# Performance work log

Measured on AMD Instinct MI355X. Metric: run time of the kernel, lower is better.

Reference implementation:

```python
import jax, jax.numpy as jnp
import numpy as np

EPS = 1e-5
LAMBDA_REG = 1.0
ALPHA_ENTROPY = 0.5
ALPHA_DIVERSITY = 0.5

B, N, D, K = 32, 1024, 256, 512  # batch, tokens, dim_embed, num_embed


def setup_inputs() -> dict:
    key = jax.random.key(0)
    k0, k1, k2 = jax.random.split(key, 3)
    inputs = jax.random.normal(k0, (B, N, D), dtype=jnp.float32)
    gamma = jnp.ones((D,), jnp.float32)
    beta = jnp.zeros((D,), jnp.float32)
    # keras 'uniform' initializer default: U(-0.05, 0.05)
    embed_w = jax.random.uniform(k1, (D, K), jnp.float32, -0.05, 0.05)
    # keras 'random_normal' default: stddev=0.05
    d_w = jax.random.normal(k2, (D, D), jnp.float32) * 0.05
    d_b = jnp.zeros((D,), jnp.float32)
    return {"inputs": inputs, "gamma": gamma, "beta": beta,
            "embed_w": embed_w, "d_w": d_w, "d_b": d_b}


def _project_columns_to_simplex(P_sol):
    # P_sol: (K, M); project each column onto the probability simplex.
    P_t = P_sol.T                                   # (M, K)
    sorted_P = -jnp.sort(-P_t, axis=1)              # descending
    cumsum = jnp.cumsum(sorted_P, axis=1)
    k = jnp.arange(1, K + 1, dtype=P_t.dtype)
    thresholds = (cumsum - 1.0) / k
    valid = (sorted_P > thresholds).astype(jnp.int32)
    max_idx = jnp.argmax(valid * jnp.arange(K, dtype=jnp.int32), axis=1)  # (M,)
    sel_cumsum = jnp.take_along_axis(cumsum, max_idx[:, None], axis=1)[:, 0]
    theta = (sel_cumsum - 1.0) / (max_idx.astype(P_t.dtype) + 1.0)
    return jax.nn.relu(P_t - theta[:, None]).T      # (K, M)


def _forward(inputs, gamma, beta, embed_w, d_w, d_b):
    # dense + layernorm
    x = jnp.matmul(inputs, d_w) + d_b
    mean = jnp.mean(x, axis=-1, keepdims=True)
    var = jnp.var(x, axis=-1, keepdims=True)
    x = gamma * ((x - mean) / jnp.sqrt(var + EPS)) + beta

    flat = x.reshape(-1, D)                          # (M, D)
    flat_sg = jax.lax.stop_gradient(flat)

    # hard assignment (VQ-style, on detached encodings)
    dists = (jnp.sum(flat_sg ** 2, axis=1, keepdims=True)
             + jnp.sum(embed_w ** 2, axis=0, keepdims=True)
             - 2.0 * jnp.matmul(flat_sg, embed_w))   # (M, K)
    assign = jnp.argmin(dists, axis=1)
    P_tilde = jax.nn.one_hot(assign, K, dtype=jnp.float32).T  # (K, M)

    # regularized least squares: (C^T C + lam I) P = C^T Z + lam P_tilde
    C = embed_w                                       # (D, K)
    Z = flat.T                                        # (D, M)
    A = jnp.matmul(C.T, C) + LAMBDA_REG * jnp.eye(K, dtype=jnp.float32)
    b = jnp.matmul(C.T, Z) + LAMBDA_REG * P_tilde     # (K, M)
    P_sol = jnp.linalg.solve(A, b)
    P_proj = _project_columns_to_simplex(P_sol)       # (K, M)

    out_P_proj = P_proj.T.reshape(B, N, K)

    # perplexity
    p_j = jnp.mean(out_P_proj, axis=(0, 1))
    p_j = jnp.clip(p_j, 1e-10, 1.0 - 1e-9)
    p_j = p_j / jnp.sum(p_j)
    entropy_bits = -jnp.sum(p_j * jnp.log(p_j) / jnp.log(2.0))
    perplexity = jnp.power(2.0, entropy_bits)

    Zq_flat = jnp.matmul(C, P_proj).T                 # (M, D)

    # entropy regularizer
    p_mean = jnp.mean(out_P_proj, axis=(0, 1))
    p_mn = p_mean / (jnp.sum(p_mean) + EPS)
    entropy_reg = -jnp.sum(p_mn * jnp.log(p_mn + EPS))

    # diversity loss on l2-normalized codebook columns
    norm_cb = embed_w / jnp.sqrt(jnp.maximum(jnp.sum(embed_w ** 2, axis=0, keepdims=True), 1e-12))
    sims = jnp.matmul(norm_cb.T, norm_cb)
    masked = sims * (1.0 - jnp.eye(K, dtype=jnp.float32))
    diversity_loss = jnp.mean(jax.nn.relu(masked))

    primary_loss = jnp.mean((Zq_flat - flat) ** 2)  # discrete_loss=False path
    loss = primary_loss + ALPHA_ENTROPY * entropy_reg + ALPHA_DIVERSITY * diversity_loss

    Zq = Zq_flat.reshape(B, N, D)
    return Zq, out_P_proj, loss, perplexity


def reference(inputs, gamma, beta, embed_w, d_w, d_b):
    return _forward(inputs, gamma, beta, embed_w, d_w, d_b)
```

## Files before the change

kernel.cpp:

```cpp
#include <hip/hip_runtime.h>
#include <math.h>


#define M_ 32768
#define D_ 256
#define K_ 512
#define TAU 0.006f

typedef short bf16x8 __attribute__((ext_vector_type(8)));
typedef unsigned short u16x8 __attribute__((ext_vector_type(8)));
typedef unsigned short u16x4 __attribute__((ext_vector_type(4)));
typedef float f32x4 __attribute__((ext_vector_type(4)));

#define LSTR 56

__device__ inline void split_rne(float f, unsigned short& h, unsigned short& l)
{
    unsigned int u = __float_as_uint(f);
    unsigned int uh = u + (0x7FFFu + ((u >> 16) & 1u));
    h = (unsigned short)(uh >> 16);
    float fh = __uint_as_float(((unsigned int)h) << 16);
    float r = f - fh;
    l = (unsigned short)(__float_as_uint(r) >> 16);
}

__device__ inline unsigned short rne16(float f)
{
    unsigned int u = __float_as_uint(f);
    u += 0x7FFFu + ((u >> 16) & 1u);
    return (unsigned short)(u >> 16);
}

__device__ inline void stage16r(const float* __restrict__ g,
                                unsigned short* __restrict__ lh)
{
    unsigned short hi[16];
#pragma unroll
    for (int q = 0; q < 4; ++q) {
        float4 v = ((const float4*)g)[q];
        float f[4] = {v.x, v.y, v.z, v.w};
#pragma unroll
        for (int e = 0; e < 4; ++e) hi[q*4+e] = rne16(f[e]);
    }
    *(u16x8*)lh       = *(u16x8*)hi;
    *(u16x8*)(lh + 8) = *(u16x8*)(hi + 8);
}

template<int EPI, int AU16>
__global__ __launch_bounds__(256)
void mfma_gemm(const float* __restrict__ Af, const unsigned short* __restrict__ Ah,
               const unsigned short* __restrict__ Bh,
               float* __restrict__ Out, int Kd, int N,
               const float* __restrict__ AinvM, const int* __restrict__ assign,
               const float* Zref, float* __restrict__ lossPart)
{
    __shared__ unsigned short sA[128*LSTR];
    __shared__ unsigned short sB[128*LSTR];
    __shared__ float red[256];
    const int tid = threadIdx.x;
    const int m0 = blockIdx.y * 128, n0 = blockIdx.x * 128;
    const int w = tid >> 6, lane = tid & 63;
    const int wr = (w & 1) * 64, wc = (w >> 1) * 64;
    const int cg = lane >> 4, cr = lane & 15;

    f32x4 acc[4][4];
    const f32x4 z4 = {0.f, 0.f, 0.f, 0.f};
#pragma unroll
    for (int i = 0; i < 4; ++i)
#pragma unroll
        for (int j = 0; j < 4; ++j) acc[i][j] = z4;

    const int sr = tid >> 1;
    const int sk = (tid & 1) * 16;
    const int soff = sr * LSTR + sk;
    const unsigned short* Bgh = Bh + (size_t)(n0 + sr) * Kd + sk;

    for (int kb = 0; kb < Kd; kb += 32) {
        if (AU16) {
            const unsigned short* Agh = Ah + (size_t)(m0 + sr) * Kd + sk + kb;
            *(u16x8*)&sA[soff]     = *(const u16x8*)(Agh);
            *(u16x8*)&sA[soff + 8] = *(const u16x8*)(Agh + 8);
        } else {
            stage16r(Af + (size_t)(m0 + sr) * Kd + sk + kb, sA + soff);
        }
        *(u16x8*)&sB[soff]     = *(const u16x8*)(Bgh + kb);
        *(u16x8*)&sB[soff + 8] = *(const u16x8*)(Bgh + kb + 8);
        __syncthreads();
        bf16x8 ah[4], bh[4];
#pragma unroll
        for (int f = 0; f < 4; ++f) {
            ah[f] = *(const bf16x8*)&sA[(wr + f*16 + cr) * LSTR + cg*8];
            bh[f] = *(const bf16x8*)&sB[(wc + f*16 + cr) * LSTR + cg*8];
        }
#pragma unroll
        for (int i = 0; i < 4; ++i)
#pragma unroll
            for (int j = 0; j < 4; ++j)
                acc[i][j] = __builtin_amdgcn_mfma_f32_16x16x32_bf16(ah[i], bh[j], acc[i][j], 0, 0, 0);
        __syncthreads();
    }

    if (EPI == 2) {
#pragma unroll
        for (int i = 0; i < 4; ++i) {
#pragma unroll
            for (int q = 0; q < 4; ++q) {
                const int row = m0 + wr + i*16 + cg*4 + q;
                const int am = assign[row];
                const float* Arow = AinvM + (size_t)am * K_ + n0 + wc;
#pragma unroll
                for (int j = 0; j < 4; ++j)
                    Out[(size_t)row * N + n0 + wc + j*16 + cr] =
                        acc[i][j][q] + Arow[j*16 + cr];
            }
        }
    } else {
        float lsum = 0.f;
#pragma unroll
        for (int i = 0; i < 4; ++i) {
#pragma unroll
            for (int q = 0; q < 4; ++q) {
                const int row = m0 + wr + i*16 + cg*4 + q;
#pragma unroll
                for (int j = 0; j < 4; ++j) {
                    const int col = n0 + wc + j*16 + cr;
                    const float v = acc[i][j][q];
                    const float zv = Zref[(size_t)row * N + col];
                    const float d = v - zv;
                    lsum += d * d;
                    Out[(size_t)row * N + col] = v;
                }
            }
        }
        red[tid] = lsum;
        __syncthreads();
        for (int s = 128; s > 0; s >>= 1) {
            if (tid < s) red[tid] += red[tid + s];
            __syncthreads();
        }
        if (tid == 0) lossPart[blockIdx.y * gridDim.x + blockIdx.x] = red[0];
    }
}

__global__ __launch_bounds__(256)
void score_mfma_argmin(const unsigned short* __restrict__ Zh, const unsigned short* __restrict__ Zl,
                       const unsigned short* __restrict__ Bth, const unsigned short* __restrict__ Btl,
                       const float* __restrict__ cn2, const float* __restrict__ zn2,
                       float* __restrict__ PV, float* __restrict__ PB,
                       int* __restrict__ PI)
{
    __shared__ unsigned short sAh[128*LSTR], sAl[128*LSTR];
    __shared__ unsigned short sBh[128*LSTR], sBl[128*LSTR];
    __shared__ float l1v[128][2], l2v[128][2];
    __shared__ int   liv[128][2];
    const int tid = threadIdx.x;
    const int m0 = blockIdx.y * 128, n0 = blockIdx.x * 128;
    const int w = tid >> 6, lane = tid & 63;
    const int wr = (w & 1) * 64, wc = (w >> 1) * 64;
    const int cg = lane >> 4, cr = lane & 15;

    f32x4 acc[4][4];
    const f32x4 z4 = {0.f, 0.f, 0.f, 0.f};
#pragma unroll
    for (int i = 0; i < 4; ++i)
#pragma unroll
        for (int j = 0; j < 4; ++j) acc[i][j] = z4;

    const int sr = tid >> 1;
    const int sk = (tid & 1) * 16;
    const int soff = sr * LSTR + sk;
    const unsigned short* Ah = Zh  + (size_t)(m0 + sr) * D_ + sk;
    const unsigned short* Al = Zl  + (size_t)(m0 + sr) * D_ + sk;
    const unsigned short* Bh = Bth + (size_t)(n0 + sr) * D_ + sk;
    const unsigned short* Bl = Btl + (size_t)(n0 + sr) * D_ + sk;

    for (int kb = 0; kb < D_; kb += 32) {
        *(u16x8*)&sAh[soff]     = *(const u16x8*)(Ah + kb);
        *(u16x8*)&sAh[soff + 8] = *(const u16x8*)(Ah + kb + 8);
        *(u16x8*)&sAl[soff]     = *(const u16x8*)(Al + kb);
        *(u16x8*)&sAl[soff + 8] = *(const u16x8*)(Al + kb + 8);
        *(u16x8*)&sBh[soff]     = *(const u16x8*)(Bh + kb);
        *(u16x8*)&sBh[soff + 8] = *(const u16x8*)(Bh + kb + 8);
        *(u16x8*)&sBl[soff]     = *(const u16x8*)(Bl + kb);
        *(u16x8*)&sBl[soff + 8] = *(const u16x8*)(Bl + kb + 8);
        __syncthreads();
        bf16x8 ah[4], al[4], bh[4], bl[4];
#pragma unroll
        for (int f = 0; f < 4; ++f) {
            const int ao = (wr + f*16 + cr) * LSTR + cg*8;
            ah[f] = *(const bf16x8*)&sAh[ao];
            al[f] = *(const bf16x8*)&sAl[ao];
            const int bo = (wc + f*16 + cr) * LSTR + cg*8;
            bh[f] = *(const bf16x8*)&sBh[bo];
            bl[f] = *(const bf16x8*)&sBl[bo];
        }
#pragma unroll
        for (int i = 0; i < 4; ++i)
#pragma unroll
            for (int j = 0; j < 4; ++j) {
                acc[i][j] = __builtin_amdgcn_mfma_f32_16x16x32_bf16(ah[i], bh[j], acc[i][j], 0, 0, 0);
                acc[i][j] = __builtin_amdgcn_mfma_f32_16x16x32_bf16(al[i], bh[j], acc[i][j], 0, 0, 0);
                acc[i][j] = __builtin_amdgcn_mfma_f32_16x16x32_bf16(ah[i], bl[j], acc[i][j], 0, 0, 0);
            }
        __syncthreads();
    }

    const int half = wc >> 6;
#pragma unroll
    for (int i = 0; i < 4; ++i) {
#pragma unroll
        for (int q = 0; q < 4; ++q) {
            const int rl = wr + i*16 + cg*4 + q;
            const float zr = zn2[m0 + rl];
            float b1 = 3.4e38f, b2 = 3.4e38f; int i1 = 0x7fffffff;
#pragma unroll
            for (int j = 0; j < 4; ++j) {
                const int col = n0 + wc + j*16 + cr;
                const float d = (zr + cn2[col]) - 2.0f * acc[i][j][q];
                if (d < b1 || (d == b1 && col < i1)) { b2 = b1; b1 = d; i1 = col; }
                else if (d < b2) b2 = d;
            }
#pragma unroll
            for (int off = 1; off < 16; off <<= 1) {
                const float o1 = __shfl_xor(b1, off);
                const int   oi = __shfl_xor(i1, off);
                const float o2 = __shfl_xor(b2, off);
                if (o1 < b1 || (o1 == b1 && oi < i1)) { b2 = fminf(b1, o2); b1 = o1; i1 = oi; }
                else { b2 = fminf(o1, b2); }
            }
            if (cr == 0) { l1v[rl][half] = b1; l2v[rl][half] = b2; liv[rl][half] = i1; }
        }
    }
    __syncthreads();
    if (tid < 128) {
        const float a1 = l1v[tid][0], a2 = l2v[tid][0]; const int ai = liv[tid][0];
        const float c1 = l1v[tid][1], c2 = l2v[tid][1]; const int ci = liv[tid][1];
        float b1, b2; int bi;
        if (c1 < a1 || (c1 == a1 && ci < ai)) { b1 = c1; bi = ci; b2 = fminf(a1, c2); }
        else { b1 = a1; bi = ai; b2 = fminf(c1, a2); }
        const size_t o = (size_t)(m0 + tid) * 4 + blockIdx.x;
        PV[o] = b1; PB[o] = b2; PI[o] = bi;
    }
}

__global__ void argmin_reduce4(const float* __restrict__ PV, const float* __restrict__ PB,
                               const int* __restrict__ PI, int* __restrict__ assign,
                               int* __restrict__ rlist, int* __restrict__ rcount)
{
    const int m = blockIdx.x * 256 + threadIdx.x;
    float b1 = PV[(size_t)m*4], b2 = PB[(size_t)m*4]; int i1 = PI[(size_t)m*4];
#pragma unroll
    for (int s = 1; s < 4; ++s) {
        const float o1 = PV[(size_t)m*4+s], o2 = PB[(size_t)m*4+s];
        const int oi = PI[(size_t)m*4+s];
        if (o1 < b1 || (o1 == b1 && oi < i1)) { b2 = fminf(b1, o2); b1 = o1; i1 = oi; }
        else { b2 = fminf(o1, b2); }
    }
    assign[m] = i1;
    if (b2 - b1 < TAU) { const int p = atomicAdd(rcount, 1); rlist[p] = m; }
}

__global__ __launch_bounds__(256)
void repair_gemm(const float* __restrict__ Z, const float* __restrict__ B,
                 const float* __restrict__ cn2, const float* __restrict__ zn2,
                 const int* __restrict__ rlist, const int* __restrict__ rcount,
                 float* __restrict__ PV, int* __restrict__ PI)
{
    const int n = rcount[0];
    const int m0 = blockIdx.y * 128;
    if (m0 >= n) return;
    __shared__ float As[16][132];
    __shared__ float Bs[16][128];
    __shared__ int rows_s[128];
    const int tid = threadIdx.x;
    const int tx = tid & 15, ty = tid >> 4;
    const int n0 = blockIdx.x * 128;

    if (tid < 128) rows_s[tid] = (m0 + tid < n) ? rlist[m0 + tid] : rlist[0];
    __syncthreads();

    float acc[8][8];
#pragma unroll
    for (int i = 0; i < 8; ++i)
#pragma unroll
        for (int j = 0; j < 8; ++j) acc[i][j] = 0.f;

    const int ar = tid >> 1, ac = (tid & 1) * 8;
    const int br = tid >> 4, bc = (tid & 15) * 8;
    const float* Ap = Z + (size_t)rows_s[ar] * D_ + ac;
    const float* Bp = B + (size_t)br * K_ + n0 + bc;

    for (int kb = 0; kb < D_; kb += 16) {
        float4 a0 = *(const float4*)(Ap + kb);
        float4 a1 = *(const float4*)(Ap + kb + 4);
        float4 b0 = *(const float4*)(Bp + (size_t)kb * K_);
        float4 b1 = *(const float4*)(Bp + (size_t)kb * K_ + 4);
        As[ac+0][ar] = a0.x; As[ac+1][ar] = a0.y; As[ac+2][ar] = a0.z; As[ac+3][ar] = a0.w;
        As[ac+4][ar] = a1.x; As[ac+5][ar] = a1.y; As[ac+6][ar] = a1.z; As[ac+7][ar] = a1.w;
        *(float4*)&Bs[br][bc]     = b0;
        *(float4*)&Bs[br][bc + 4] = b1;
        __syncthreads();
#pragma unroll
        for (int kk = 0; kk < 16; ++kk) {
            float4 av0 = *(const float4*)&As[kk][ty*4];
            float4 av1 = *(const float4*)&As[kk][64 + ty*4];
            float4 bv0 = *(const float4*)&Bs[kk][tx*4];
            float4 bv1 = *(const float4*)&Bs[kk][64 + tx*4];
            float a_[8] = {av0.x, av0.y, av0.z, av0.w, av1.x, av1.y, av1.z, av1.w};
            float b_[8] = {bv0.x, bv0.y, bv0.z, bv0.w, bv1.x, bv1.y, bv1.z, bv1.w};
#pragma unroll
            for (int i = 0; i < 8; ++i)
#pragma unroll
                for (int j = 0; j < 8; ++j)
                    acc[i][j] = fmaf(a_[i], b_[j], acc[i][j]);
        }
        __syncthreads();
    }

#pragma unroll
    for (int hi = 0; hi < 2; ++hi) {
#pragma unroll
        for (int i = 0; i < 4; ++i) {
            const int rl = hi*64 + ty*4 + i;
            if (m0 + rl >= n) continue;
            const float zr = zn2[rows_s[rl]];
            float best = 3.4e38f; int bi = 0x7fffffff;
#pragma unroll
            for (int hj = 0; hj < 2; ++hj) {
#pragma unroll
                for (int j = 0; j < 4; ++j) {
                    const int col = n0 + hj*64 + tx*4 + j;
                    const float t1 = zr + cn2[col];
                    const float d  = t1 - 2.0f * acc[hi*4+i][hj*4+j];
                    if (d < best) { best = d; bi = col; }
                }
            }
#pragma unroll
            for (int off = 1; off < 16; off <<= 1) {
                const float ov = __shfl_xor(best, off);
                const int   oi = __shfl_xor(bi, off);
                if (ov < best || (ov == best && oi < bi)) { best = ov; bi = oi; }
            }
            if (tx == 0) {
                PV[(size_t)(m0 + rl) * 4 + blockIdx.x] = best;
                PI[(size_t)(m0 + rl) * 4 + blockIdx.x] = bi;
            }
        }
    }
}

__global__ void repair_scatter(const float* __restrict__ PV, const int* __restrict__ PI,
                               const int* __restrict__ rlist, const int* __restrict__ rcount,
                               int* __restrict__ assign)
{
    const int r = blockIdx.x * 256 + threadIdx.x;
    if (r >= rcount[0]) return;
    float best = PV[(size_t)r * 4]; int bi = PI[(size_t)r * 4];
#pragma unroll
    for (int nb = 1; nb < 4; ++nb) {
        const float v = PV[(size_t)r * 4 + nb]; const int ix = PI[(size_t)r * 4 + nb];
        if (v < best || (v == best && ix < bi)) { best = v; bi = ix; }
    }
    assign[rlist[r]] = bi;
}

__global__ __launch_bounds__(256)
void dense_ln_kernel(const float* __restrict__ A, const float* __restrict__ Bw,
                     const float* __restrict__ bias, const float* __restrict__ gamma,
                     const float* __restrict__ beta, float* __restrict__ Z,
                     float* __restrict__ zn2,
                     unsigned short* __restrict__ Zh, unsigned short* __restrict__ Zl)
{
    __shared__ float As[16][36];
    __shared__ float Bs[16][256];
    __shared__ float rred[32][17];
    __shared__ float rstat[32];
    const int tid = threadIdx.x, tx = tid & 15, ty = tid >> 4;
    const int m0 = blockIdx.x * 32;
    float acc[2][16];
#pragma unroll
    for (int i = 0; i < 2; ++i)
#pragma unroll
        for (int j = 0; j < 16; ++j) acc[i][j] = 0.f;

    const int ar = tid >> 2, ac = (tid & 3) * 4;
    const int br = tid >> 4, bc = (tid & 15) * 16;
    for (int kb = 0; kb < 256; kb += 16) {
        if (tid < 128) {
            float4 a = *(const float4*)(A + (size_t)(m0 + ar) * 256 + kb + ac);
            As[ac+0][ar] = a.x; As[ac+1][ar] = a.y; As[ac+2][ar] = a.z; As[ac+3][ar] = a.w;
        }
#pragma unroll
        for (int q = 0; q < 4; ++q)
            *(float4*)&Bs[br][bc + q*4] =
                *(const float4*)(Bw + (size_t)(kb + br) * 256 + bc + q*4);
        __syncthreads();
#pragma unroll
        for (int kk = 0; kk < 16; ++kk) {
            float av[2] = {As[kk][ty*2], As[kk][ty*2 + 1]};
            float bv[16];
#pragma unroll
            for (int q = 0; q < 4; ++q) {
                float4 b4 = *(const float4*)&Bs[kk][q*64 + tx*4];
                bv[q*4+0] = b4.x; bv[q*4+1] = b4.y; bv[q*4+2] = b4.z; bv[q*4+3] = b4.w;
            }
#pragma unroll
            for (int i = 0; i < 2; ++i)
#pragma unroll
                for (int j = 0; j < 16; ++j)
                    acc[i][j] = fmaf(av[i], bv[j], acc[i][j]);
        }
        __syncthreads();
    }

    float bcol[16];
#pragma unroll
    for (int q = 0; q < 4; ++q) {
        float4 b4 = *(const float4*)(bias + q*64 + tx*4);
        bcol[q*4+0] = b4.x; bcol[q*4+1] = b4.y; bcol[q*4+2] = b4.z; bcol[q*4+3] = b4.w;
    }
#pragma unroll
    for (int i = 0; i < 2; ++i)
#pragma unroll
        for (int j = 0; j < 16; ++j) acc[i][j] += bcol[j];

#pragma unroll
    for (int i = 0; i < 2; ++i) {
        float s = 0.f;
#pragma unroll
        for (int j = 0; j < 16; ++j) s += acc[i][j];
        rred[ty*2+i][tx] = s;
    }
    __syncthreads();
    if (tid < 32) {
        float s = 0.f;
#pragma unroll
        for (int t = 0; t < 16; ++t) s += rred[tid][t];
        rstat[tid] = s * (1.f / 256.f);
    }
    __syncthreads();
    float mean_[2];
#pragma unroll
    for (int i = 0; i < 2; ++i) mean_[i] = rstat[ty*2+i];

#pragma unroll
    for (int i = 0; i < 2; ++i) {
        float s = 0.f;
#pragma unroll
        for (int j = 0; j < 16; ++j) { float d = acc[i][j] - mean_[i]; s += d * d; }
        rred[ty*2+i][tx] = s;
    }
    __syncthreads();
    if (tid < 32) {
        float s = 0.f;
#pragma unroll
        for (int t = 0; t < 16; ++t) s += rred[tid][t];
        rstat[tid] = s * (1.f / 256.f);
    }
    __syncthreads();
    float rstd_[2];
#pragma unroll
    for (int i = 0; i < 2; ++i) rstd_[i] = sqrtf(rstat[ty*2+i] + 1e-5f);

    float gam[16], bet[16];
#pragma unroll
    for (int q = 0; q < 4; ++q) {
        float4 g4 = *(const float4*)(gamma + q*64 + tx*4);
        float4 e4 = *(const float4*)(beta  + q*64 + tx*4);
        gam[q*4+0] = g4.x; gam[q*4+1] = g4.y; gam[q*4+2] = g4.z; gam[q*4+3] = g4.w;
        bet[q*4+0] = e4.x; bet[q*4+1] = e4.y; bet[q*4+2] = e4.z; bet[q*4+3] = e4.w;
    }
#pragma unroll
    for (int i = 0; i < 2; ++i)
#pragma unroll
        for (int j = 0; j < 16; ++j) {
            const float d = acc[i][j] - mean_[i];
            acc[i][j] = gam[j] * (d / rstd_[i]) + bet[j];
        }

#pragma unroll
    for (int i = 0; i < 2; ++i) {
        float s = 0.f;
#pragma unroll
        for (int j = 0; j < 16; ++j) s += acc[i][j] * acc[i][j];
        rred[ty*2+i][tx] = s;
    }
    __syncthreads();
    if (tid < 32) {
        float s = 0.f;
#pragma unroll
        for (int t = 0; t < 16; ++t) s += rred[tid][t];
        zn2[m0 + tid] = s;
    }

#pragma unroll
    for (int i = 0; i < 2; ++i) {
        const int row = m0 + ty*2 + i;
#pragma unroll
        for (int q = 0; q < 4; ++q) {
            float4 v;
            v.x = acc[i][q*4+0]; v.y = acc[i][q*4+1];
            v.z = acc[i][q*4+2]; v.w = acc[i][q*4+3];
            const size_t pos = (size_t)row * 256 + q*64 + tx*4;
            *(float4*)(Z + pos) = v;
            unsigned short h[4], l[4];
            split_rne(v.x, h[0], l[0]); split_rne(v.y, h[1], l[1]);
            split_rne(v.z, h[2], l[2]); split_rne(v.w, h[3], l[3]);
            *(u16x4*)(Zh + pos) = *(u16x4*)h;
            *(u16x4*)(Zl + pos) = *(u16x4*)l;
        }
    }
}

template<int TRA, int ASUM, int BSUM>
__global__ __launch_bounds__(256)
void sk_gemm(const float* __restrict__ A, const float* __restrict__ B,
             float* __restrict__ Out, int M, int N, int Kd)
{
    __shared__ float As[16][68];
    __shared__ float Bs[16][68];
    const int tid = threadIdx.x;
    const int tx = tid & 15, ty = tid >> 4;
    const int n0 = blockIdx.x * 64, m0 = blockIdx.y * 64;
    const int kw = Kd >> 2;
    const int kb0 = blockIdx.z * kw;
    const size_t aP = (size_t)M * Kd;
    const size_t bP = (size_t)Kd * N;
    float acc[4][4];
#pragma unroll
    for (int i = 0; i < 4; ++i)
#pragma unroll
        for (int j = 0; j < 4; ++j) acc[i][j] = 0.f;

    for (int kb = kb0; kb < kb0 + kw; kb += 16) {
        if (TRA == 0) {
            const int ar2 = tid >> 2, ac2 = (tid & 3) * 4;
            const size_t off = (size_t)(m0 + ar2) * Kd + kb + ac2;
            float4 a;
            if (ASUM) {
                float4 a0 = *(const float4*)(A + off);
                float4 a1 = *(const float4*)(A + aP + off);
                float4 a2 = *(const float4*)(A + 2*aP + off);
                float4 a3 = *(const float4*)(A + 3*aP + off);
                a.x = a0.x + a1.x + a2.x + a3.x;
                a.y = a0.y + a1.y + a2.y + a3.y;
                a.z = a0.z + a1.z + a2.z + a3.z;
                a.w = a0.w + a1.w + a2.w + a3.w;
                if (ASUM == 2) {
                    const int row = m0 + ar2, colb = kb + ac2;
                    if (row == colb)     a.x += 1.f;
                    if (row == colb + 1) a.y += 1.f;
                    if (row == colb + 2) a.z += 1.f;
                    if (row == colb + 3) a.w += 1.f;
                }
            } else {
                a = *(const float4*)(A + off);
            }
            As[ac2+0][ar2] = a.x; As[ac2+1][ar2] = a.y;
            As[ac2+2][ar2] = a.z; As[ac2+3][ar2] = a.w;
        } else {
            const int ar2 = tid >> 4, ac2 = (tid & 15) * 4;
            float4 a = *(const float4*)(A + (size_t)(kb + ar2) * M + m0 + ac2);
            *(float4*)&As[ar2][ac2] = a;
        }
        {
            const int br2 = tid >> 4, bc2 = (tid & 15) * 4;
            const size_t off = (size_t)(kb + br2) * N + n0 + bc2;
            float4 b;
            if (BSUM) {
                float4 b0 = *(const float4*)(B + off);
                float4 b1 = *(const float4*)(B + bP + off);
                float4 b2 = *(const float4*)(B + 2*bP + off);
                float4 b3 = *(const float4*)(B + 3*bP + off);
                b.x = b0.x + b1.x + b2.x + b3.x;
                b.y = b0.y + b1.y + b2.y + b3.y;
                b.z = b0.z + b1.z + b2.z + b3.z;
                b.w = b0.w + b1.w + b2.w + b3.w;
            } else {
                b = *(const float4*)(B + off);
            }
            *(float4*)&Bs[br2][bc2] = b;
        }
        __syncthreads();
#pragma unroll
        for (int kk = 0; kk < 16; ++kk) {
            float4 a4 = *(const float4*)&As[kk][ty*4];
            float4 b4 = *(const float4*)&Bs[kk][tx*4];
            float a_[4] = {a4.x, a4.y, a4.z, a4.w};
            float b_[4] = {b4.x, b4.y, b4.z, b4.w};
#pragma unroll
            for (int i = 0; i < 4; ++i)
#pragma unroll
                for (int j = 0; j < 4; ++j)
                    acc[i][j] = fmaf(a_[i], b_[j], acc[i][j]);
        }
        __syncthreads();
    }
    float* Op = Out + (size_t)blockIdx.z * M * N;
#pragma unroll
    for (int i = 0; i < 4; ++i)
#pragma unroll
        for (int j = 0; j < 4; ++j)
            Op[(size_t)(m0 + ty*4 + i) * N + n0 + tx*4 + j] = acc[i][j];
}

__global__ void xn_reduce(const float* __restrict__ Xc, const float* __restrict__ Xp,
                          float* __restrict__ Xn)
{
    const int idx = blockIdx.x * 256 + threadIdx.x;
    const float s = Xp[idx] + Xp[65536 + idx] + Xp[131072 + idx] + Xp[196608 + idx];
    Xn[idx] = 2.f * Xc[idx] - s;
}

__global__ void ainv_reduce(const float* __restrict__ Ap, float* __restrict__ Ainv)
{
    const int idx = blockIdx.x * 256 + threadIdx.x;
    const int i = idx >> 9, j = idx & 511;
    const float s = Ap[idx] + Ap[262144 + idx] + Ap[524288 + idx] + Ap[786432 + idx];
    Ainv[idx] = ((i == j) ? 1.f : 0.f) - s;
}

__global__ void g_reduce(const float* __restrict__ Gp, const float* __restrict__ cn2,
                         float* __restrict__ divPart)
{
    __shared__ float red[256];
    __shared__ float rsn[512];
    const int t = threadIdx.x;
    rsn[t]       = 1.f / sqrtf(fmaxf(cn2[t], 1e-12f));
    rsn[t + 256] = 1.f / sqrtf(fmaxf(cn2[t + 256], 1e-12f));
    __syncthreads();
    float dsum = 0.f;
#pragma unroll
    for (int e = 0; e < 4; ++e) {
        const int idx = blockIdx.x * 1024 + e * 256 + t;
        const int i = idx >> 9, j = idx & 511;
        const float g = Gp[idx] + Gp[262144 + idx] + Gp[524288 + idx] + Gp[786432 + idx];
        if (i != j) dsum += fmaxf(g * rsn[i] * rsn[j], 0.f);
    }
    red[t] = dsum; __syncthreads();
    for (int s = 128; s > 0; s >>= 1) {
        if (t < s) red[t] += red[t + s];
        __syncthreads();
    }
    if (t == 0) divPart[blockIdx.x] = red[0];
}

__global__ void rowabs_kernel(const float* __restrict__ Sp, float* __restrict__ rowAbs)
{
    __shared__ float red[256];
    const int r = blockIdx.x, t = threadIdx.x;
    const int idx = r * 256 + t;
    float v = Sp[idx] + Sp[65536 + idx] + Sp[131072 + idx] + Sp[196608 + idx];
    if (r == t) v += 1.f;
    red[t] = fabsf(v); __syncthreads();
    for (int s = 128; s > 0; s >>= 1) {
        if (t < s) red[t] += red[t + s];
        __syncthreads();
    }
    if (t == 0) rowAbs[r] = red[0];
}

__global__ void x0_init(const float* __restrict__ rowAbs, float* __restrict__ X)
{
    __shared__ float red[256];
    const int t = threadIdx.x;
    red[t] = rowAbs[t]; __syncthreads();
    for (int s = 128; s > 0; s >>= 1) {
        if (t < s) red[t] = fmaxf(red[t], red[t + s]);
        __syncthreads();
    }
    const float c = 2.f / (1.f + red[0]);
    const int idx = blockIdx.x * 256 + t;
    const int i = idx >> 8, j = idx & 255;
    X[idx] = (i == j) ? c : 0.f;
}

__global__ void ut_reduce(const float* __restrict__ Up, unsigned short* __restrict__ Uth)
{
    const int idx = blockIdx.x * 256 + threadIdx.x;
    Uth[idx] = rne16(Up[idx] + Up[131072 + idx] + Up[262144 + idx] + Up[393216 + idx]);
}

__global__ void transpose_ct(const float* __restrict__ C, float* __restrict__ Ct,
                             unsigned short* __restrict__ Cth, unsigned short* __restrict__ Ctl)
{
    const int idx = blockIdx.x * 256 + threadIdx.x;
    const int k = idx >> 8, d = idx & 255;
    const float v = C[(size_t)d * K_ + k];
    Ct[idx] = v;
    unsigned short h, l;
    split_rne(v, h, l);
    Cth[idx] = h; Ctl[idx] = l;
}

__global__ void c_native(const float* __restrict__ C, unsigned short* __restrict__ Ch)
{
    const int idx = blockIdx.x * 256 + threadIdx.x;
    Ch[idx] = rne16(C[idx]);
}

__global__ void cn2_kernel(const float* __restrict__ C, float* __restrict__ cn2)
{
    const int k = blockIdx.x * 256 + threadIdx.x;
    float s = 0.f;
    for (int d = 0; d < D_; ++d) { float c = C[(size_t)d * K_ + k]; s = fmaf(c, c, s); }
    cn2[k] = s;
}

__global__ __launch_bounds__(256)
void project_kernel(float* P)
{
    const int wave = threadIdx.x >> 6;
    const int lane = threadIdx.x & 63;
    const int row = blockIdx.x * 4 + wave;
    const size_t base = (size_t)row * K_ + lane;
    float v[8];
#pragma unroll
    for (int j = 0; j < 8; ++j) v[j] = P[base + j * 64];

    float s = 0.f;
#pragma unroll
    for (int j = 0; j < 8; ++j) s += v[j];
    for (int off = 32; off > 0; off >>= 1) s += __shfl_xor(s, off);

    float theta = (s - 1.f) * (1.f / 512.f);
    int cnt = K_;
    for (int it = 0; it < K_; ++it) {
        float ls = 0.f; int lc = 0;
#pragma unroll
        for (int j = 0; j < 8; ++j)
            if (v[j] > theta) { ls += v[j]; ++lc; }
        for (int off = 32; off > 0; off >>= 1) {
            ls += __shfl_xor(ls, off);
            lc += __shfl_xor(lc, off);
        }
        if (lc == cnt) break;
        theta = (ls - 1.f) / (float)lc;
        cnt = lc;
    }
#pragma unroll
    for (int j = 0; j < 8; ++j) P[base + j * 64] = fmaxf(v[j] - theta, 0.f);
}

__global__ __launch_bounds__(512)
void colsum_kernel(const float* __restrict__ P, float* __restrict__ part)
{
    const int k = threadIdx.x;
    const int b = blockIdx.x;
    float s = 0.f;
    const size_t base = (size_t)b * 128 * K_ + k;
    for (int r = 0; r < 128; ++r) s += P[base + (size_t)r * K_];
    part[(size_t)b * K_ + k] = s;
}

#define BLOCK_REDUCE_512(val, result) \
    red[t] = (val); __syncthreads(); \
    for (int s_ = 256; s_ > 0; s_ >>= 1) { if (t < s_) red[t] += red[t + s_]; __syncthreads(); } \
    result = red[0]; __syncthreads();

__global__ __launch_bounds__(512)
void finalize_kernel(const float* __restrict__ part, const float* __restrict__ divPart,
                     const float* __restrict__ lossPart, float* __restrict__ out_scal)
{
    __shared__ float red[512];
    const int t = threadIdx.x;

    float praw = 0.f;
    for (int b = 0; b < 256; ++b) praw += part[b * K_ + t];
    const float pm = praw * (1.f / 32768.f);

    const float pj = fminf(fmaxf(pm, 1e-10f), 1.0f);
    float sp; BLOCK_REDUCE_512(pj, sp);
    const float pjn = pj / sp;
    float Hbits; BLOCK_REDUCE_512(-pjn * logf(pjn) / 0.69314718056f, Hbits);

    float spm; BLOCK_REDUCE_512(pm, spm);
    const float s2 = spm + 1e-5f;
    const float pmn = pm / s2;
    float ereg; BLOCK_REDUCE_512(-pmn * logf(pmn + 1e-5f), ereg);

    float dv = (t < 256) ? divPart[t] : 0.f;
    float divs; BLOCK_REDUCE_512(dv, divs);
    const float divloss = divs * (1.f / 262144.f);

    float lp = lossPart[t];
    float prim; BLOCK_REDUCE_512(lp, prim);
    prim *= 1.f / 8388608.f;

    if (t == 0) {
        out_scal[0] = prim + 0.5f * ereg + 0.5f * divloss;
        out_scal[1] = exp2f(Hbits);
    }
}

extern "C" void kernel_launch(void* const* d_in, const int* in_sizes, int n_in,
                              void* d_out, int out_size, void* d_ws, size_t ws_size,
                              hipStream_t stream)
{
    const float* inputs = (const float*)d_in[0];
    const float* gamma  = (const float*)d_in[1];
    const float* beta   = (const float*)d_in[2];
    const float* C      = (const float*)d_in[3];
    const float* d_w    = (const float*)d_in[4];
    const float* d_b    = (const float*)d_in[5];

    float* out = (float*)d_out;
    float* Z = out;
    float* P = out + (size_t)M_ * D_;
    float* out_scal = P + (size_t)M_ * K_;

    float* w = (float*)d_ws;
    float* Sp   = w;     w += 4 * 65536;
    float* Tp   = w;     w += 4 * 65536;
    float* Xp   = w;     w += 4 * 65536;
    float* Up   = w;     w += 4 * 131072;
    float* Ap   = w;     w += 4 * 262144;
    float* Xa   = w;     w += 65536;
    float* Xb   = w;     w += 65536;
    float* Ainv = w;     w += 262144;
    float* Ct   = w;     w += 131072;
    float* cn2  = w;     w += 512;
    float* rowAbs = w;   w += 256;
    float* zn2  = w;     w += M_;
    float* part = w;     w += 256 * K_;
    float* lossPart = w; w += 512;
    float* divPart  = w; w += 256;
    float* PV   = w;     w += M_ * 4;
    float* PB   = w;     w += M_ * 4;
    int* PI     = (int*)w; w += M_ * 4;
    int* rlist  = (int*)w; w += M_;
    int* rcount = (int*)w; w += 16;
    int* assign = (int*)w; w += M_;
    unsigned short* Zh  = (unsigned short*)w; w += M_ * D_ / 2;
    unsigned short* Zl  = (unsigned short*)w; w += M_ * D_ / 2;
    unsigned short* Cth = (unsigned short*)w; w += (K_ * D_) / 2;
    unsigned short* Ctl = (unsigned short*)w; w += (K_ * D_) / 2;
    unsigned short* Ch  = (unsigned short*)w; w += (K_ * D_) / 2;
    unsigned short* Uth = (unsigned short*)w; w += (K_ * D_) / 2;

    hipMemsetAsync(rcount, 0, sizeof(int), stream);

    dense_ln_kernel<<<M_/32, 256, 0, stream>>>(inputs, d_w, d_b, gamma, beta, Z, zn2, Zh, Zl);
    transpose_ct<<<(K_ * D_) / 256, 256, 0, stream>>>(C, Ct, Cth, Ctl);
    c_native<<<(K_ * D_) / 256, 256, 0, stream>>>(C, Ch);
    cn2_kernel<<<K_ / 256, 256, 0, stream>>>(C, cn2);
    sk_gemm<1, 0, 0><<<dim3(4, 4, 4), 256, 0, stream>>>(Ct, Ct, Sp, 256, 256, 512);
    rowabs_kernel<<<256, 256, 0, stream>>>(Sp, rowAbs);
    x0_init<<<256, 256, 0, stream>>>(rowAbs, Xa);
    float* Xc = Xa; float* Xn = Xb;
    for (int it = 0; it < 5; ++it) {
        sk_gemm<0, 2, 0><<<dim3(4, 4, 4), 256, 0, stream>>>(Sp, Xc, Tp, 256, 256, 256);
        sk_gemm<0, 0, 1><<<dim3(4, 4, 4), 256, 0, stream>>>(Xc, Tp, Xp, 256, 256, 256);
        xn_reduce<<<256, 256, 0, stream>>>(Xc, Xp, Xn);
        float* tmp = Xc; Xc = Xn; Xn = tmp;
    }
    sk_gemm<1, 0, 0><<<dim3(4, 8, 4), 256, 0, stream>>>(C, Xc, Up, 512, 256, 256);
    sk_gemm<0, 1, 0><<<dim3(8, 8, 4), 256, 0, stream>>>(Up, C, Ap, 512, 512, 256);
    ainv_reduce<<<1024, 256, 0, stream>>>(Ap, Ainv);
    sk_gemm<1, 0, 0><<<dim3(8, 8, 4), 256, 0, stream>>>(C, C, Ap, 512, 512, 256);
    g_reduce<<<256, 256, 0, stream>>>(Ap, cn2, divPart);
    ut_reduce<<<512, 256, 0, stream>>>(Up, Uth);
    score_mfma_argmin<<<dim3(K_/128, M_/128), 256, 0, stream>>>(Zh, Zl, Cth, Ctl, cn2, zn2, PV, PB, PI);
    argmin_reduce4<<<M_/256, 256, 0, stream>>>(PV, PB, PI, assign, rlist, rcount);
    repair_gemm<<<dim3(K_/128, M_/128), 256, 0, stream>>>(Z, C, cn2, zn2, rlist, rcount, PV, PI);
    repair_scatter<<<M_/256, 256, 0, stream>>>(PV, PI, rlist, rcount, assign);
    mfma_gemm<2, 1><<<dim3(K_/128, M_/128), 256, 0, stream>>>(
        nullptr, Zh, Uth, P, D_, K_, Ainv, assign, nullptr, nullptr);
    project_kernel<<<M_/4, 256, 0, stream>>>(P);
    colsum_kernel<<<256, 512, 0, stream>>>(P, part);
    mfma_gemm<3, 0><<<dim3(D_/128, M_/128), 256, 0, stream>>>(
        P, nullptr, Ch, Z, K_, D_, nullptr, nullptr, Z, lossPart);
    finalize_kernel<<<1, 512, 0, stream>>>(part, divPart, lossPart, out_scal);

    (void)in_sizes; (void)n_in; (void)out_size; (void)ws_size;
}
```

Measured before the change: 441.7 us.

## Fuse simplex projection with column sums and enlarge dense+LN row tile

Measured after the change: 432.4 us. -2.1%, faster.

```diff
diff --git a/kernel.cpp b/kernel.cpp
--- a/kernel.cpp
+++ b/kernel.cpp
@@ -371,25 +371,23 @@
                      float* __restrict__ zn2,
                      unsigned short* __restrict__ Zh, unsigned short* __restrict__ Zl)
 {
-    __shared__ float As[16][36];
-    __shared__ float Bs[16][256];
-    __shared__ float rred[32][17];
-    __shared__ float rstat[32];
+    __shared__ float As[16][68];
+    __shared__ float Bs[16][260];
+    __shared__ float rred[64][17];
+    __shared__ float rstat[64];
     const int tid = threadIdx.x, tx = tid & 15, ty = tid >> 4;
-    const int m0 = blockIdx.x * 32;
-    float acc[2][16];
-#pragma unroll
-    for (int i = 0; i < 2; ++i)
+    const int m0 = blockIdx.x * 64;
+    float acc[4][16];
+#pragma unroll
+    for (int i = 0; i < 4; ++i)
 #pragma unroll
         for (int j = 0; j < 16; ++j) acc[i][j] = 0.f;
 
     const int ar = tid >> 2, ac = (tid & 3) * 4;
     const int br = tid >> 4, bc = (tid & 15) * 16;
     for (int kb = 0; kb < 256; kb += 16) {
-        if (tid < 128) {
-            float4 a = *(const float4*)(A + (size_t)(m0 + ar) * 256 + kb + ac);
-            As[ac+0][ar] = a.x; As[ac+1][ar] = a.y; As[ac+2][ar] = a.z; As[ac+3][ar] = a.w;
-        }
+        float4 a = *(const float4*)(A + (size_t)(m0 + ar) * 256 + kb + ac);
+        As[ac+0][ar] = a.x; As[ac+1][ar] = a.y; As[ac+2][ar] = a.z; As[ac+3][ar] = a.w;
 #pragma unroll
         for (int q = 0; q < 4; ++q)
             *(float4*)&Bs[br][bc + q*4] =
@@ -397,7 +395,8 @@
         __syncthreads();
 #pragma unroll
         for (int kk = 0; kk < 16; ++kk) {
-            float av[2] = {As[kk][ty*2], As[kk][ty*2 + 1]};
+            float4 a4 = *(const float4*)&As[kk][ty*4];
+            float av[4] = {a4.x, a4.y, a4.z, a4.w};
             float bv[16];
 #pragma unroll
             for (int q = 0; q < 4; ++q) {
@@ -405,7 +404,7 @@
                 bv[q*4+0] = b4.x; bv[q*4+1] = b4.y; bv[q*4+2] = b4.z; bv[q*4+3] = b4.w;
             }
 #pragma unroll
-            for (int i = 0; i < 2; ++i)
+            for (int i = 0; i < 4; ++i)
 #pragma unroll
                 for (int j = 0; j < 16; ++j)
                     acc[i][j] = fmaf(av[i], bv[j], acc[i][j]);
@@ -420,47 +419,47 @@
         bcol[q*4+0] = b4.x; bcol[q*4+1] = b4.y; bcol[q*4+2] = b4.z; bcol[q*4+3] = b4.w;
     }
 #pragma unroll
-    for (int i = 0; i < 2; ++i)
+    for (int i = 0; i < 4; ++i)
 #pragma unroll
         for (int j = 0; j < 16; ++j) acc[i][j] += bcol[j];
 
 #pragma unroll
-    for (int i = 0; i < 2; ++i) {
+    for (int i = 0; i < 4; ++i) {
         float s = 0.f;
 #pragma unroll
         for (int j = 0; j < 16; ++j) s += acc[i][j];
-        rred[ty*2+i][tx] = s;
+        rred[ty*4+i][tx] = s;
     }
     __syncthreads();
-    if (tid < 32) {
+    if (tid < 64) {
         float s = 0.f;
 #pragma unroll
         for (int t = 0; t < 16; ++t) s += rred[tid][t];
         rstat[tid] = s * (1.f / 256.f);
     }
     __syncthreads();
-    float mean_[2];
-#pragma unroll
-    for (int i = 0; i < 2; ++i) mean_[i] = rstat[ty*2+i];
-
-#pragma unroll
-    for (int i = 0; i < 2; ++i) {
+    float mean_[4];
+#pragma unroll
+    for (int i = 0; i < 4; ++i) mean_[i] = rstat[ty*4+i];
+
+#pragma unroll
+    for (int i = 0; i < 4; ++i) {
         float s = 0.f;
 #pragma unroll
         for (int j = 0; j < 16; ++j) { float d = acc[i][j] - mean_[i]; s += d * d; }
-        rred[ty*2+i][tx] = s;
+        rred[ty*4+i][tx] = s;
     }
     __syncthreads();
-    if (tid < 32) {
+    if (tid < 64) {
         float s = 0.f;
 #pragma unroll
         for (int t = 0; t < 16; ++t) s += rred[tid][t];
         rstat[tid] = s * (1.f / 256.f);
     }
     __syncthreads();
-    float rstd_[2];
-#pragma unroll
-    for (int i = 0; i < 2; ++i) rstd_[i] = sqrtf(rstat[ty*2+i] + 1e-5f);
+    float rstd_[4];
+#pragma unroll
+    for (int i = 0; i < 4; ++i) rstd_[i] = sqrtf(rstat[ty*4+i] + 1e-5f);
 
     float gam[16], bet[16];
 #pragma unroll
@@ -471,7 +470,7 @@
         bet[q*4+0] = e4.x; bet[q*4+1] = e4.y; bet[q*4+2] = e4.z; bet[q*4+3] = e4.w;
     }
 #pragma unroll
-    for (int i = 0; i < 2; ++i)
+    for (int i = 0; i < 4; ++i)
 #pragma unroll
         for (int j = 0; j < 16; ++j) {
             const float d = acc[i][j] - mean_[i];
@@ -479,14 +478,14 @@
         }
 
 #pragma unroll
-    for (int i = 0; i < 2; ++i) {
+    for (int i = 0; i < 4; ++i) {
         float s = 0.f;
 #pragma unroll
         for (int j = 0; j < 16; ++j) s += acc[i][j] * acc[i][j];
-        rred[ty*2+i][tx] = s;
+        rred[ty*4+i][tx] = s;
     }
     __syncthreads();
-    if (tid < 32) {
+    if (tid < 64) {
         float s = 0.f;
 #pragma unroll
         for (int t = 0; t < 16; ++t) s += rred[tid][t];
@@ -494,8 +493,8 @@
     }
 
 #pragma unroll
-    for (int i = 0; i < 2; ++i) {
-        const int row = m0 + ty*2 + i;
+    for (int i = 0; i < 4; ++i) {
+        const int row = m0 + ty*4 + i;
 #pragma unroll
         for (int q = 0; q < 4; ++q) {
             float4 v;
@@ -707,50 +706,59 @@
     cn2[k] = s;
 }
 
-__global__ __launch_bounds__(256)
-void project_kernel(float* P)
-{
+__global__ __launch_bounds__(1024)
+void project_colsum_kernel(float* P, float* __restrict__ part)
+{
+    __shared__ float ps[16][512];
     const int wave = threadIdx.x >> 6;
     const int lane = threadIdx.x & 63;
-    const int row = blockIdx.x * 4 + wave;
-    const size_t base = (size_t)row * K_ + lane;
-    float v[8];
-#pragma unroll
-    for (int j = 0; j < 8; ++j) v[j] = P[base + j * 64];
-
-    float s = 0.f;
-#pragma unroll
-    for (int j = 0; j < 8; ++j) s += v[j];
-    for (int off = 32; off > 0; off >>= 1) s += __shfl_xor(s, off);
-
-    float theta = (s - 1.f) * (1.f / 512.f);
-    int cnt = K_;
-    for (int it = 0; it < K_; ++it) {
-        float ls = 0.f; int lc = 0;
-#pragma unroll
-        for (int j = 0; j < 8; ++j)
-            if (v[j] > theta) { ls += v[j]; ++lc; }
-        for (int off = 32; off > 0; off >>= 1) {
-            ls += __shfl_xor(ls, off);
-            lc += __shfl_xor(lc, off);
-        }
-        if (lc == cnt) break;
-        theta = (ls - 1.f) / (float)lc;
-        cnt = lc;
-    }
-#pragma unroll
-    for (int j = 0; j < 8; ++j) P[base + j * 64] = fmaxf(v[j] - theta, 0.f);
-}
-
-__global__ __launch_bounds__(512)
-void colsum_kernel(const float* __restrict__ P, float* __restrict__ part)
-{
-    const int k = threadIdx.x;
-    const int b = blockIdx.x;
-    float s = 0.f;
-    const size_t base = (size_t)b * 128 * K_ + k;
-    for (int r = 0; r < 128; ++r) s += P[base + (size_t)r * K_];
-    part[(size_t)b * K_ + k] = s;
+    float psum[8];
+#pragma unroll
+    for (int j = 0; j < 8; ++j) psum[j] = 0.f;
+
+    for (int r = 0; r < 8; ++r) {
+        const int row = blockIdx.x * 128 + wave * 8 + r;
+        const size_t base = (size_t)row * K_ + lane;
+        float v[8];
+#pragma unroll
+        for (int j = 0; j < 8; ++j) v[j] = P[base + j * 64];
+
+        float s = 0.f;
+#pragma unroll
+        for (int j = 0; j < 8; ++j) s += v[j];
+        for (int off = 32; off > 0; off >>= 1) s += __shfl_xor(s, off);
+
+        float theta = (s - 1.f) * (1.f / 512.f);
+        int cnt = K_;
+        for (int it = 0; it < K_; ++it) {
+            float ls = 0.f; int lc = 0;
+#pragma unroll
+            for (int j = 0; j < 8; ++j)
+                if (v[j] > theta) { ls += v[j]; ++lc; }
+            for (int off = 32; off > 0; off >>= 1) {
+                ls += __shfl_xor(ls, off);
+                lc += __shfl_xor(lc, off);
+            }
+            if (lc == cnt) break;
+            theta = (ls - 1.f) / (float)lc;
+            cnt = lc;
+        }
+#pragma unroll
+        for (int j = 0; j < 8; ++j) {
+            const float o = fmaxf(v[j] - theta, 0.f);
+            P[base + j * 64] = o;
+            psum[j] += o;
+        }
+    }
+#pragma unroll
+    for (int j = 0; j < 8; ++j) ps[wave][lane + j * 64] = psum[j];
+    __syncthreads();
+    for (int c = threadIdx.x; c < 512; c += 1024) {
+        float s = 0.f;
+#pragma unroll
+        for (int wv = 0; wv < 16; ++wv) s += ps[wv][c];
+        part[(size_t)blockIdx.x * K_ + c] = s;
+    }
 }
 
 #define BLOCK_REDUCE_512(val, result) \
@@ -840,7 +848,7 @@
 
     hipMemsetAsync(rcount, 0, sizeof(int), stream);
 
-    dense_ln_kernel<<<M_/32, 256, 0, stream>>>(inputs, d_w, d_b, gamma, beta, Z, zn2, Zh, Zl);
+    dense_ln_kernel<<<M_/64, 256, 0, stream>>>(inputs, d_w, d_b, gamma, beta, Z, zn2, Zh, Zl);
     transpose_ct<<<(K_ * D_) / 256, 256, 0, stream>>>(C, Ct, Cth, Ctl);
     c_native<<<(K_ * D_) / 256, 256, 0, stream>>>(C, Ch);
     cn2_kernel<<<K_ / 256, 256, 0, stream>>>(C, cn2);
@@ -866,8 +874,7 @@
     repair_scatter<<<M_/256, 256, 0, stream>>>(PV, PI, rlist, rcount, assign);
     mfma_gemm<2, 1><<<dim3(K_/128, M_/128), 256, 0, stream>>>(
         nullptr, Zh, Uth, P, D_, K_, Ainv, assign, nullptr, nullptr);
-    project_kernel<<<M_/4, 256, 0, stream>>>(P);
-    colsum_kernel<<<256, 512, 0, stream>>>(P, part);
+    project_colsum_kernel<<<M_/128, 1024, 0, stream>>>(P, part);
     mfma_gemm<3, 0><<<dim3(D_/128, M_/128), 256, 0, stream>>>(
         P, nullptr, Ch, Z, K_, D_, nullptr, nullptr, Z, lossPart);
     finalize_kernel<<<1, 512, 0, stream>>>(part, divPart, lossPart, out_scal);
```
